# Optimization experiments

Measured on AMD Instinct MI355X. Metric: run time of the kernel, lower is better.

The kernel has to match this reference:

```python
import jax, jax.numpy as jnp
import numpy as np

HEADS = 16
DIM_HEAD = 64
SCALE = DIM_HEAD ** (-0.5)


def setup_inputs() -> dict:
    key = jax.random.key(0)
    ks = jax.random.split(key, 6)
    B, N, D = 2, 2048, 1024
    inner = HEADS * DIM_HEAD  # 1024
    s = 0.02
    return {
        "x": jax.random.normal(ks[0], (B, N, D), dtype=jnp.float32),
        "Wq": jax.random.normal(ks[1], (D, inner), dtype=jnp.float32) * s,
        "Wk": jax.random.normal(ks[2], (D, inner), dtype=jnp.float32) * s,
        "Wv": jax.random.normal(ks[3], (D, inner), dtype=jnp.float32) * s,
        "Wo": jax.random.normal(ks[4], (inner, D), dtype=jnp.float32) * s,
        "bo": jnp.zeros((D,), dtype=jnp.float32),
    }


def reference(x, Wq, Wk, Wv, Wo, bo):
    B, N, _ = x.shape
    # projections, split heads: [B, N, inner] -> [B, H, N, d]
    def split(t):
        return t.reshape(B, N, HEADS, DIM_HEAD).transpose(0, 2, 1, 3)
    q = split(x @ Wq)
    k = split(x @ Wk)  # self-attention: context = x
    v = split(x @ Wv)
    # scores [B, H, N, N], softmax over keys
    scores = jnp.einsum('bhid,bhjd->bhij', q, k) * SCALE
    attn = jax.nn.softmax(scores, axis=-1)
    out = jnp.einsum('bhij,bhjd->bhid', attn, v)
    out = out.transpose(0, 2, 1, 3).reshape(B, N, HEADS * DIM_HEAD)
    return out @ Wo + bo
```

## Files before the change

### kernel.cpp

```cpp
#include <hip/hip_runtime.h>
#include <hip/hip_bf16.h>
#include <stdint.h>

typedef unsigned short u16;
typedef __attribute__((ext_vector_type(8))) short bf16x8;
typedef __attribute__((ext_vector_type(4))) float f32x4;
typedef __attribute__((ext_vector_type(4))) unsigned int u32x4;

#define QSCALE 0.18033688011112042f

__device__ __forceinline__ u16 f2bf(float f) {
  return __builtin_bit_cast(u16, __float2bfloat16(f));
}

__device__ __forceinline__ uint32_t pkcvt(float a, float b) {
  return (uint32_t)f2bf(a) | ((uint32_t)f2bf(b) << 16);
}

__device__ __forceinline__ void gll16(const void* g, void* l) {
  __builtin_amdgcn_global_load_lds(
      (__attribute__((address_space(1))) void*)(uintptr_t)g,
      (__attribute__((address_space(3))) void*)l, 16, 0, 0);
}

__global__ __launch_bounds__(256)
void cvt_all_kernel(const float* __restrict__ x,
                    const float* __restrict__ Wq, const float* __restrict__ Wk,
                    const float* __restrict__ Wv, const float* __restrict__ Wo,
                    u16* __restrict__ xb, u16* __restrict__ Wqkvt, u16* __restrict__ Wot) {
  __shared__ float tile[32][33];
  const int bid = blockIdx.x, tid = threadIdx.x;
  if (bid < 4096) {
    const int z = bid >> 10, xy = bid & 1023;
    const float* src = (z == 0) ? Wq : (z == 1) ? Wk : (z == 2) ? Wv : Wo;
    const float scale = (z == 0) ? QSCALE : 1.0f;
    u16* dst = (z == 3) ? Wot : (Wqkvt + (size_t)z * 1024 * 1024);
    const int n0 = (xy & 31) * 32, k0 = (xy >> 5) * 32;
    const int tx = tid & 31, ty = tid >> 5;
#pragma unroll
    for (int i = 0; i < 4; ++i)
      tile[ty * 4 + i][tx] = src[(size_t)(k0 + ty * 4 + i) * 1024 + n0 + tx];
    __syncthreads();
#pragma unroll
    for (int i = 0; i < 4; ++i)
      dst[(size_t)(n0 + ty * 4 + i) * 1024 + k0 + tx] = f2bf(tile[tx][ty * 4 + i] * scale);
  } else {
    size_t i = (size_t)(bid - 4096) * 256 + tid;
    const float4* p = (const float4*)x + i * 2;
    float4 a = p[0], b = p[1];
    ushort4 lo, hi;
    lo.x = f2bf(a.x); lo.y = f2bf(a.y); lo.z = f2bf(a.z); lo.w = f2bf(a.w);
    hi.x = f2bf(b.x); hi.y = f2bf(b.y); hi.z = f2bf(b.z); hi.w = f2bf(b.w);
    ((ushort4*)xb)[i * 2]     = lo;
    ((ushort4*)xb)[i * 2 + 1] = hi;
  }
}

__global__ __launch_bounds__(256)
void gemm_qkv_kernel(const u16* __restrict__ A, const u16* __restrict__ Bt,
                     u16* __restrict__ Qb, u16* __restrict__ Kb, u16* __restrict__ Vtb) {
  __shared__ __align__(16) u16 As[128 * 64];
  __shared__ __align__(16) u16 Bs[128 * 64];
  const int row0 = blockIdx.x * 128, col0 = blockIdx.y * 128;
  const int tid = threadIdx.x, lane = tid & 63, wid = tid >> 6;
  const int wr = (wid >> 1) * 64, wc = (wid & 1) * 64;
  const int lr = lane & 15, lg = lane >> 4;
  const int swz = (lr & 7) << 4;

  f32x4 acc[4][4];
#pragma unroll
  for (int m = 0; m < 4; ++m)
#pragma unroll
    for (int n = 0; n < 4; ++n) acc[m][n] = (f32x4){0.f, 0.f, 0.f, 0.f};

  for (int k0 = 0; k0 < 1024; k0 += 64) {
    __syncthreads();
#pragma unroll
    for (int i = 0; i < 4; ++i) {
      const int c = tid + i * 256;
      const int row = c >> 3;
      const int sc = ((c & 7) * 16) ^ ((row & 7) << 4);
      gll16((const char*)A  + ((size_t)(row0 + row) * 1024 + k0) * 2 + sc, (char*)As + c * 16);
      gll16((const char*)Bt + ((size_t)(col0 + row) * 1024 + k0) * 2 + sc, (char*)Bs + c * 16);
    }
    __syncthreads();
    bf16x8 af[4][2], bfr[4][2];
#pragma unroll
    for (int s = 0; s < 2; ++s) {
#pragma unroll
      for (int m = 0; m < 4; ++m)
        af[m][s] = *(const bf16x8*)((const char*)As + (wr + m * 16 + lr) * 128 + ((s * 64 + lg * 16) ^ swz));
#pragma unroll
      for (int n = 0; n < 4; ++n)
        bfr[n][s] = *(const bf16x8*)((const char*)Bs + (wc + n * 16 + lr) * 128 + ((s * 64 + lg * 16) ^ swz));
    }
#pragma unroll
    for (int m = 0; m < 4; ++m)
#pragma unroll
      for (int n = 0; n < 4; ++n)
#pragma unroll
        for (int s = 0; s < 2; ++s)
          acc[m][n] = __builtin_amdgcn_mfma_f32_16x16x32_bf16(af[m][s], bfr[n][s], acc[m][n], 0, 0, 0);
  }

#pragma unroll
  for (int m = 0; m < 4; ++m) {
#pragma unroll
    for (int n = 0; n < 4; ++n) {
      const int gcol = col0 + wc + n * 16 + lr;
      const int w = gcol >> 10, rem = gcol & 1023;
      const int h = rem >> 6, dd = rem & 63;
      const int grow0 = row0 + wr + m * 16 + lg * 4;
      if (w == 2) {
        const int b0 = grow0 >> 11, nn0 = grow0 & 2047;
        const int kin = nn0 & 63;
        const int kp = (kin & 32) | ((kin & 12) << 1) | ((kin & 16) >> 2);
        ushort4 sv;
        sv.x = f2bf(acc[m][n][0]); sv.y = f2bf(acc[m][n][1]);
        sv.z = f2bf(acc[m][n][2]); sv.w = f2bf(acc[m][n][3]);
        *(ushort4*)&Vtb[((size_t)(b0 * 16 + h) * 64 + dd) * 2048 + (nn0 & ~63) + kp] = sv;
      } else {
#pragma unroll
        for (int r = 0; r < 4; ++r) {
          const int grow = grow0 + r;
          const int b = grow >> 11, nn = grow & 2047;
          const int bh = b * 16 + h;
          const u16 hv = f2bf(acc[m][n][r]);
          if (w == 0) Qb[((size_t)bh * 2048 + nn) * 64 + dd] = hv;
          else        Kb[((size_t)bh * 2048 + nn) * 64 + dd] = hv;
        }
      }
    }
  }
}

__global__ __launch_bounds__(256, 2)
void attn_kernel(const u16* __restrict__ Qb, const u16* __restrict__ Kb,
                 const u16* __restrict__ Vtb, u16* __restrict__ Ob) {
  __shared__ __align__(16) u16 Ks[2][128 * 64];
  __shared__ __align__(16) u16 Vs[2][128 * 64];
  const int tid = threadIdx.x, lane = tid & 63, wid = tid >> 6;
  const int bid = blockIdx.x;
  const int vv = (bid & 7) * 64 + (bid >> 3);
  const int qt = vv & 15, bh = vv >> 4;
  const int lr = lane & 15, lg = lane >> 4;

  const u16* Qp = Qb + ((size_t)bh * 2048 + qt * 128 + wid * 32) * 64;
  const char* Kg = (const char*)(Kb + (size_t)bh * 2048 * 64);
  const char* Vg = (const char*)(Vtb + (size_t)bh * 64 * 2048);

  bf16x8 aq[2][2];
#pragma unroll
  for (int qc = 0; qc < 2; ++qc)
#pragma unroll
    for (int ks = 0; ks < 2; ++ks)
      aq[qc][ks] = *(const bf16x8*)&Qp[(qc * 16 + lr) * 64 + ks * 32 + lg * 8];

  auto stage = [&](int buf, int kv0) {
#pragma unroll
    for (int i = 0; i < 4; ++i) {
      const int c = tid + i * 256;
      const int row = c >> 3;
      const int sc = ((c & 7) * 16) ^ ((row & 7) << 4);
      gll16(Kg + (size_t)(kv0 + row) * 128 + sc, (char*)Ks[buf] + c * 16);
      gll16(Vg + (size_t)(row & 63) * 4096 + (size_t)(kv0 + (row >> 6) * 64) * 2 + sc,
            (char*)Vs[buf] + c * 16);
    }
  };

  const int swz = (lr & 7) << 4;
  const int xk0 = (lg * 16) ^ swz;
  const int xk1 = (64 + lg * 16) ^ swz;

  f32x4 acco[4][2];
#pragma unroll
  for (int ct = 0; ct < 4; ++ct)
#pragma unroll
    for (int qc = 0; qc < 2; ++qc) acco[ct][qc] = (f32x4){0.f, 0.f, 0.f, 0.f};
  f32x4 lacc[2];
  lacc[0] = (f32x4){0.f, 0.f, 0.f, 0.f};
  lacc[1] = (f32x4){0.f, 0.f, 0.f, 0.f};
  const f32x4 minit = (f32x4){-8.f, -8.f, -8.f, -8.f};
  u32x4 ow;
  ow.x = ow.y = ow.z = ow.w = 0x3F803F80u;
  const bf16x8 ones = __builtin_bit_cast(bf16x8, ow);

  stage(0, 0);
  asm volatile("s_waitcnt vmcnt(0)" ::: "memory");
  __syncthreads();

  int buf = 0;
  for (int t = 0; t < 16; ++t) {
    if (t < 15) stage(buf ^ 1, (t + 1) * 128);
#pragma unroll
    for (int u = 0; u < 2; ++u) {
      const char* kbase = (const char*)Ks[buf] + u * 8192 + lr * 128;
      const char* vbase = (const char*)Vs[buf] + u * 8192 + lr * 128;

      bf16x8 kf[4][2];
#pragma unroll
      for (int kt = 0; kt < 4; ++kt) {
        kf[kt][0] = *(const bf16x8*)(kbase + kt * 2048 + xk0);
        kf[kt][1] = *(const bf16x8*)(kbase + kt * 2048 + xk1);
      }
      f32x4 s[4][2];
      __builtin_amdgcn_s_setprio(1);
#pragma unroll
      for (int kt = 0; kt < 4; ++kt)
#pragma unroll
        for (int qc = 0; qc < 2; ++qc) {
          f32x4 tacc = __builtin_amdgcn_mfma_f32_16x16x32_bf16(kf[kt][0], aq[qc][0], minit, 0, 0, 0);
          s[kt][qc]  = __builtin_amdgcn_mfma_f32_16x16x32_bf16(kf[kt][1], aq[qc][1], tacc, 0, 0, 0);
        }
      __builtin_amdgcn_s_setprio(0);
      bf16x8 pa[2][2];
#pragma unroll
      for (int qc = 0; qc < 2; ++qc) {
#pragma unroll
        for (int kt = 0; kt < 4; ++kt)
#pragma unroll
          for (int r = 0; r < 4; ++r)
            s[kt][qc][r] = __builtin_amdgcn_exp2f(s[kt][qc][r]);
#pragma unroll
        for (int ks = 0; ks < 2; ++ks) {
          u32x4 w;
          w.x = pkcvt(s[2 * ks][qc][0],     s[2 * ks][qc][1]);
          w.y = pkcvt(s[2 * ks][qc][2],     s[2 * ks][qc][3]);
          w.z = pkcvt(s[2 * ks + 1][qc][0], s[2 * ks + 1][qc][1]);
          w.w = pkcvt(s[2 * ks + 1][qc][2], s[2 * ks + 1][qc][3]);
          pa[qc][ks] = __builtin_bit_cast(bf16x8, w);
        }
        lacc[qc] = __builtin_amdgcn_mfma_f32_16x16x32_bf16(ones, pa[qc][0], lacc[qc], 0, 0, 0);
        lacc[qc] = __builtin_amdgcn_mfma_f32_16x16x32_bf16(ones, pa[qc][1], lacc[qc], 0, 0, 0);
      }
      __builtin_amdgcn_s_setprio(1);
#pragma unroll
      for (int ct = 0; ct < 4; ++ct) {
        const char* vb = vbase + ct * 2048;
#pragma unroll
        for (int ks = 0; ks < 2; ++ks) {
          bf16x8 vf = *(const bf16x8*)(vb + ((ks * 64 + lg * 16) ^ swz));
#pragma unroll
          for (int qc = 0; qc < 2; ++qc)
            acco[ct][qc] = __builtin_amdgcn_mfma_f32_16x16x32_bf16(vf, pa[qc][ks], acco[ct][qc], 0, 0, 0);
        }
      }
      __builtin_amdgcn_s_setprio(0);
    }
    asm volatile("s_waitcnt vmcnt(0)" ::: "memory");
    __syncthreads();
    buf ^= 1;
  }

  const int b = bh >> 4, h = bh & 15;
#pragma unroll
  for (int qc = 0; qc < 2; ++qc) {
    const int q = qt * 128 + wid * 32 + qc * 16 + lr;
    const float inv = 1.0f / lacc[qc][0];
#pragma unroll
    for (int ct = 0; ct < 4; ++ct) {
      uint2 st;
      st.x = pkcvt(acco[ct][qc][0] * inv, acco[ct][qc][1] * inv);
      st.y = pkcvt(acco[ct][qc][2] * inv, acco[ct][qc][3] * inv);
      *(uint2*)&Ob[((size_t)b * 2048 + q) * 1024 + h * 64 + ct * 16 + lg * 4] = st;
    }
  }
}

__global__ __launch_bounds__(256)
void gemm_out_kernel(const u16* __restrict__ A, const u16* __restrict__ Bt,
                     const float* __restrict__ bo, float* __restrict__ out) {
  __shared__ __align__(16) u16 As[128 * 64];
  __shared__ __align__(16) u16 Bs[128 * 64];
  const int row0 = blockIdx.x * 128, col0 = blockIdx.y * 128;
  const int tid = threadIdx.x, lane = tid & 63, wid = tid >> 6;
  const int wr = (wid >> 1) * 64, wc = (wid & 1) * 64;
  const int lr = lane & 15, lg = lane >> 4;
  const int swz = (lr & 7) << 4;

  f32x4 acc[4][4];
#pragma unroll
  for (int m = 0; m < 4; ++m)
#pragma unroll
    for (int n = 0; n < 4; ++n) acc[m][n] = (f32x4){0.f, 0.f, 0.f, 0.f};

  for (int k0 = 0; k0 < 1024; k0 += 64) {
    __syncthreads();
#pragma unroll
    for (int i = 0; i < 4; ++i) {
      const int c = tid + i * 256;
      const int row = c >> 3;
      const int sc = ((c & 7) * 16) ^ ((row & 7) << 4);
      gll16((const char*)A  + ((size_t)(row0 + row) * 1024 + k0) * 2 + sc, (char*)As + c * 16);
      gll16((const char*)Bt + ((size_t)(col0 + row) * 1024 + k0) * 2 + sc, (char*)Bs + c * 16);
    }
    __syncthreads();
    bf16x8 af[4][2], bfr[4][2];
#pragma unroll
    for (int s = 0; s < 2; ++s) {
#pragma unroll
      for (int m = 0; m < 4; ++m)
        af[m][s] = *(const bf16x8*)((const char*)As + (wr + m * 16 + lr) * 128 + ((s * 64 + lg * 16) ^ swz));
#pragma unroll
      for (int n = 0; n < 4; ++n)
        bfr[n][s] = *(const bf16x8*)((const char*)Bs + (wc + n * 16 + lr) * 128 + ((s * 64 + lg * 16) ^ swz));
    }
#pragma unroll
    for (int m = 0; m < 4; ++m)
#pragma unroll
      for (int n = 0; n < 4; ++n)
#pragma unroll
        for (int s = 0; s < 2; ++s)
          acc[m][n] = __builtin_amdgcn_mfma_f32_16x16x32_bf16(af[m][s], bfr[n][s], acc[m][n], 0, 0, 0);
  }

#pragma unroll
  for (int m = 0; m < 4; ++m) {
#pragma unroll
    for (int n = 0; n < 4; ++n) {
      const int gcol = col0 + wc + n * 16 + lr;
      const float bv = bo[gcol];
#pragma unroll
      for (int r = 0; r < 4; ++r) {
        const int grow = row0 + wr + m * 16 + lg * 4 + r;
        out[(size_t)grow * 1024 + gcol] = acc[m][n][r] + bv;
      }
    }
  }
}

extern "C" void kernel_launch(void* const* d_in, const int* in_sizes, int n_in,
                              void* d_out, int out_size, void* d_ws, size_t ws_size,
                              hipStream_t stream) {
  const float* x  = (const float*)d_in[0];
  const float* Wq = (const float*)d_in[1];
  const float* Wk = (const float*)d_in[2];
  const float* Wv = (const float*)d_in[3];
  const float* Wo = (const float*)d_in[4];
  const float* bo = (const float*)d_in[5];
  float* out = (float*)d_out;

  char* ws = (char*)d_ws;
  u16* xb    = (u16*)(ws);
  u16* wqkvt = (u16*)(ws + ((size_t)8  << 20));
  u16* wot   = (u16*)(ws + ((size_t)14 << 20));
  u16* Qb    = (u16*)(ws + ((size_t)16 << 20));
  u16* Kb    = (u16*)(ws + ((size_t)24 << 20));
  u16* Vtb   = (u16*)(ws + ((size_t)32 << 20));
  u16* Ob    = xb;

  hipLaunchKernelGGL(cvt_all_kernel, dim3(6144), dim3(256), 0, stream,
                     x, Wq, Wk, Wv, Wo, xb, wqkvt, wot);
  hipLaunchKernelGGL(gemm_qkv_kernel, dim3(32, 24), dim3(256), 0, stream,
                     xb, wqkvt, Qb, Kb, Vtb);
  hipLaunchKernelGGL(attn_kernel, dim3(512), dim3(256), 0, stream,
                     Qb, Kb, Vtb, Ob);
  hipLaunchKernelGGL(gemm_out_kernel, dim3(32, 8), dim3(256), 0, stream,
                     Ob, wot, bo, out);
}
```

Before: 119.8 us.

## Double-buffer LDS with BK=32 in QKV and output GEMMs to overlap loads

Both projection GEMMs now use two LDS buffers with a K-step of 32 instead of a single 64-wide buffer. The next tile's global-to-LDS loads are issued before computing on the current one, so memory latency is hidden behind the MFMAs, with one barrier per iteration instead of two. The change also adds a new XOR swizzle suited to 64-byte rows and raises wave priority around the MFMA block. In exchange it doubles the iteration count, giving less work per barrier, and it still waits on vmcnt(0) each step.

```diff
diff --git a/kernel.cpp b/kernel.cpp
--- a/kernel.cpp
+++ b/kernel.cpp
@@ -59,13 +59,13 @@
 __global__ __launch_bounds__(256)
 void gemm_qkv_kernel(const u16* __restrict__ A, const u16* __restrict__ Bt,
                      u16* __restrict__ Qb, u16* __restrict__ Kb, u16* __restrict__ Vtb) {
-  __shared__ __align__(16) u16 As[128 * 64];
-  __shared__ __align__(16) u16 Bs[128 * 64];
+  __shared__ __align__(16) u16 As[2][128 * 32];
+  __shared__ __align__(16) u16 Bs[2][128 * 32];
   const int row0 = blockIdx.x * 128, col0 = blockIdx.y * 128;
   const int tid = threadIdx.x, lane = tid & 63, wid = tid >> 6;
   const int wr = (wid >> 1) * 64, wc = (wid & 1) * 64;
   const int lr = lane & 15, lg = lane >> 4;
-  const int swz = (lr & 7) << 4;
+  const int fsw = (lg ^ ((lr >> 2) & 3)) * 16;
 
   f32x4 acc[4][4];
 #pragma unroll
@@ -73,34 +73,41 @@
 #pragma unroll
     for (int n = 0; n < 4; ++n) acc[m][n] = (f32x4){0.f, 0.f, 0.f, 0.f};
 
-  for (int k0 = 0; k0 < 1024; k0 += 64) {
+  auto stage = [&](int b, int k0) {
+#pragma unroll
+    for (int i = 0; i < 2; ++i) {
+      const int c = tid + i * 256;
+      const int row = c >> 2, pos = c & 3;
+      const int sp = (pos ^ ((row >> 2) & 3)) * 16;
+      gll16((const char*)A  + ((size_t)(row0 + row) * 1024 + k0) * 2 + sp, (char*)As[b] + c * 16);
+      gll16((const char*)Bt + ((size_t)(col0 + row) * 1024 + k0) * 2 + sp, (char*)Bs[b] + c * 16);
+    }
+  };
+
+  stage(0, 0);
+  asm volatile("s_waitcnt vmcnt(0)" ::: "memory");
+  __syncthreads();
+
+  int buf = 0;
+  for (int t = 0; t < 32; ++t) {
+    if (t < 31) stage(buf ^ 1, (t + 1) * 32);
+    bf16x8 af[4], bfr[4];
+#pragma unroll
+    for (int m = 0; m < 4; ++m)
+      af[m] = *(const bf16x8*)((const char*)As[buf] + (wr + m * 16 + lr) * 64 + fsw);
+#pragma unroll
+    for (int n = 0; n < 4; ++n)
+      bfr[n] = *(const bf16x8*)((const char*)Bs[buf] + (wc + n * 16 + lr) * 64 + fsw);
+    __builtin_amdgcn_s_setprio(1);
+#pragma unroll
+    for (int m = 0; m < 4; ++m)
+#pragma unroll
+      for (int n = 0; n < 4; ++n)
+        acc[m][n] = __builtin_amdgcn_mfma_f32_16x16x32_bf16(af[m], bfr[n], acc[m][n], 0, 0, 0);
+    __builtin_amdgcn_s_setprio(0);
+    asm volatile("s_waitcnt vmcnt(0)" ::: "memory");
     __syncthreads();
-#pragma unroll
-    for (int i = 0; i < 4; ++i) {
-      const int c = tid + i * 256;
-      const int row = c >> 3;
-      const int sc = ((c & 7) * 16) ^ ((row & 7) << 4);
-      gll16((const char*)A  + ((size_t)(row0 + row) * 1024 + k0) * 2 + sc, (char*)As + c * 16);
-      gll16((const char*)Bt + ((size_t)(col0 + row) * 1024 + k0) * 2 + sc, (char*)Bs + c * 16);
-    }
-    __syncthreads();
-    bf16x8 af[4][2], bfr[4][2];
-#pragma unroll
-    for (int s = 0; s < 2; ++s) {
-#pragma unroll
-      for (int m = 0; m < 4; ++m)
-        af[m][s] = *(const bf16x8*)((const char*)As + (wr + m * 16 + lr) * 128 + ((s * 64 + lg * 16) ^ swz));
-#pragma unroll
-      for (int n = 0; n < 4; ++n)
-        bfr[n][s] = *(const bf16x8*)((const char*)Bs + (wc + n * 16 + lr) * 128 + ((s * 64 + lg * 16) ^ swz));
-    }
-#pragma unroll
-    for (int m = 0; m < 4; ++m)
-#pragma unroll
-      for (int n = 0; n < 4; ++n)
-#pragma unroll
-        for (int s = 0; s < 2; ++s)
-          acc[m][n] = __builtin_amdgcn_mfma_f32_16x16x32_bf16(af[m][s], bfr[n][s], acc[m][n], 0, 0, 0);
+    buf ^= 1;
   }
 
 #pragma unroll
@@ -270,13 +277,13 @@
 __global__ __launch_bounds__(256)
 void gemm_out_kernel(const u16* __restrict__ A, const u16* __restrict__ Bt,
                      const float* __restrict__ bo, float* __restrict__ out) {
-  __shared__ __align__(16) u16 As[128 * 64];
-  __shared__ __align__(16) u16 Bs[128 * 64];
+  __shared__ __align__(16) u16 As[2][128 * 32];
+  __shared__ __align__(16) u16 Bs[2][128 * 32];
   const int row0 = blockIdx.x * 128, col0 = blockIdx.y * 128;
   const int tid = threadIdx.x, lane = tid & 63, wid = tid >> 6;
   const int wr = (wid >> 1) * 64, wc = (wid & 1) * 64;
   const int lr = lane & 15, lg = lane >> 4;
-  const int swz = (lr & 7) << 4;
+  const int fsw = (lg ^ ((lr >> 2) & 3)) * 16;
 
   f32x4 acc[4][4];
 #pragma unroll
@@ -284,34 +291,41 @@
 #pragma unroll
     for (int n = 0; n < 4; ++n) acc[m][n] = (f32x4){0.f, 0.f, 0.f, 0.f};
 
-  for (int k0 = 0; k0 < 1024; k0 += 64) {
+  auto stage = [&](int b, int k0) {
+#pragma unroll
+    for (int i = 0; i < 2; ++i) {
+      const int c = tid + i * 256;
+      const int row = c >> 2, pos = c & 3;
+      const int sp = (pos ^ ((row >> 2) & 3)) * 16;
+      gll16((const char*)A  + ((size_t)(row0 + row) * 1024 + k0) * 2 + sp, (char*)As[b] + c * 16);
+      gll16((const char*)Bt + ((size_t)(col0 + row) * 1024 + k0) * 2 + sp, (char*)Bs[b] + c * 16);
+    }
+  };
+
+  stage(0, 0);
+  asm volatile("s_waitcnt vmcnt(0)" ::: "memory");
+  __syncthreads();
+
+  int buf = 0;
+  for (int t = 0; t < 32; ++t) {
+    if (t < 31) stage(buf ^ 1, (t + 1) * 32);
+    bf16x8 af[4], bfr[4];
+#pragma unroll
+    for (int m = 0; m < 4; ++m)
+      af[m] = *(const bf16x8*)((const char*)As[buf] + (wr + m * 16 + lr) * 64 + fsw);
+#pragma unroll
+    for (int n = 0; n < 4; ++n)
+      bfr[n] = *(const bf16x8*)((const char*)Bs[buf] + (wc + n * 16 + lr) * 64 + fsw);
+    __builtin_amdgcn_s_setprio(1);
+#pragma unroll
+    for (int m = 0; m < 4; ++m)
+#pragma unroll
+      for (int n = 0; n < 4; ++n)
+        acc[m][n] = __builtin_amdgcn_mfma_f32_16x16x32_bf16(af[m], bfr[n], acc[m][n], 0, 0, 0);
+    __builtin_amdgcn_s_setprio(0);
+    asm volatile("s_waitcnt vmcnt(0)" ::: "memory");
     __syncthreads();
-#pragma unroll
-    for (int i = 0; i < 4; ++i) {
-      const int c = tid + i * 256;
-      const int row = c >> 3;
-      const int sc = ((c & 7) * 16) ^ ((row & 7) << 4);
-      gll16((const char*)A  + ((size_t)(row0 + row) * 1024 + k0) * 2 + sc, (char*)As + c * 16);
-      gll16((const char*)Bt + ((size_t)(col0 + row) * 1024 + k0) * 2 + sc, (char*)Bs + c * 16);
-    }
-    __syncthreads();
-    bf16x8 af[4][2], bfr[4][2];
-#pragma unroll
-    for (int s = 0; s < 2; ++s) {
-#pragma unroll
-      for (int m = 0; m < 4; ++m)
-        af[m][s] = *(const bf16x8*)((const char*)As + (wr + m * 16 + lr) * 128 + ((s * 64 + lg * 16) ^ swz));
-#pragma unroll
-      for (int n = 0; n < 4; ++n)
-        bfr[n][s] = *(const bf16x8*)((const char*)Bs + (wc + n * 16 + lr) * 128 + ((s * 64 + lg * 16) ^ swz));
-    }
-#pragma unroll
-    for (int m = 0; m < 4; ++m)
-#pragma unroll
-      for (int n = 0; n < 4; ++n)
-#pragma unroll
-        for (int s = 0; s < 2; ++s)
-          acc[m][n] = __builtin_amdgcn_mfma_f32_16x16x32_bf16(af[m][s], bfr[n][s], acc[m][n], 0, 0, 0);
+    buf ^= 1;
   }
 
 #pragma unroll
```

New measurement: 116.9 us. 1.02x faster.
